# Kernel optimization log

Measured on AMD Instinct MI355X. Metric: run time of the kernel, lower is better.

The kernel has to match this reference:

```python
import jax, jax.numpy as jnp
import numpy as np

L = 4      # temporal transformer layers
H = 8      # heads
D = 512    # d_model (CLIP ViT-B/32 output dim)
FF = 2048  # feedforward dim
Q = 32     # query_pad_length
NEXP = 2   # visual expansion tokens
EPS = 1e-5


def _l2norm(x):
    n = jnp.linalg.norm(x, axis=-1, keepdims=True)
    return x / jnp.maximum(n, 1e-12)


def _layer_norm(x, w, b):
    m = jnp.mean(x, axis=-1, keepdims=True)
    v = jnp.mean(jnp.square(x - m), axis=-1, keepdims=True)
    return (x - m) / jnp.sqrt(v + EPS) * w + b


def _encoder_layer(x, Wqkv, bqkv, Wo, bo, g1, c1, W1, b1, W2, b2, g2, c2):
    # PyTorch TransformerEncoderLayer, batch_first, post-norm, ReLU, eval mode.
    B, S, _ = x.shape
    dh = D // H
    qkv = x @ Wqkv.T + bqkv                      # [B,S,3D]
    q, k, v = jnp.split(qkv, 3, axis=-1)
    q = q.reshape(B, S, H, dh).transpose(0, 2, 1, 3)
    k = k.reshape(B, S, H, dh).transpose(0, 2, 1, 3)
    v = v.reshape(B, S, H, dh).transpose(0, 2, 1, 3)
    scores = jnp.einsum('bhqd,bhkd->bhqk', q, k) / jnp.sqrt(jnp.float32(dh))
    attn = jax.nn.softmax(scores, axis=-1)
    o = jnp.einsum('bhqk,bhkd->bhqd', attn, v).transpose(0, 2, 1, 3).reshape(B, S, D)
    o = o @ Wo.T + bo
    x = _layer_norm(x + o, g1, c1)
    ff = jax.nn.relu(x @ W1.T + b1) @ W2.T + b2
    x = _layer_norm(x + ff, g2, c2)
    return x


def setup_inputs() -> dict:
    key = jax.random.key(0)
    ks = jax.random.split(key, 8)
    B, F = 256, 30
    s = 0.02
    return {
        'text_features': jax.random.normal(ks[0], (B, D), dtype=jnp.float32),
        'frame_features': jax.random.normal(ks[1], (B, F, D), dtype=jnp.float32),
        'expansion_tokens': jax.random.normal(ks[2], (1, NEXP, D), dtype=jnp.float32) * s,
        'W_qkv': jax.random.normal(ks[3], (L, 3 * D, D), dtype=jnp.float32) * s,
        'b_qkv': jnp.zeros((L, 3 * D), jnp.float32),
        'W_o': jax.random.normal(ks[4], (L, D, D), dtype=jnp.float32) * s,
        'b_o': jnp.zeros((L, D), jnp.float32),
        'ln1_w': jnp.ones((L, D), jnp.float32),
        'ln1_b': jnp.zeros((L, D), jnp.float32),
        'W1': jax.random.normal(ks[5], (L, FF, D), dtype=jnp.float32) * s,
        'b1': jnp.zeros((L, FF), jnp.float32),
        'W2': jax.random.normal(ks[6], (L, D, FF), dtype=jnp.float32) * s,
        'b2': jnp.zeros((L, D), jnp.float32),
        'ln2_w': jnp.ones((L, D), jnp.float32),
        'ln2_b': jnp.zeros((L, D), jnp.float32),
    }


def reference(text_features, frame_features, expansion_tokens, W_qkv, b_qkv,
              W_o, b_o, ln1_w, ln1_b, W1, b1, W2, b2, ln2_w, ln2_b):
    B, F = frame_features.shape[0], frame_features.shape[1]
    # encode_query: expand pooled text feature to Q identical tokens, l2-normalize
    q_feats = _l2norm(jnp.broadcast_to(text_features[:, None, :], (B, Q, D)))
    # temporal encoder on [frames; expansion tokens]
    x = jnp.concatenate(
        [frame_features, jnp.broadcast_to(expansion_tokens, (B, NEXP, D))], axis=1)
    for l in range(L):
        x = _encoder_layer(x, W_qkv[l], b_qkv[l], W_o[l], b_o[l],
                           ln1_w[l], ln1_b[l], W1[l], b1[l], W2[l], b2[l],
                           ln2_w[l], ln2_b[l])
    frame_n = _l2norm(frame_features)   # [B,F,D]
    video_n = _l2norm(x)                # [B,F+NEXP,D]
    # pairwise ColBERT MaxSim: similarities[i,j] = MMS(query_i, video_j)
    sim_f = jnp.einsum('bqd,cfd->bcqf', q_feats, frame_n).max(axis=-1).mean(axis=-1)
    sim_v = jnp.einsum('bqd,cvd->bcqv', q_feats, video_n).max(axis=-1).mean(axis=-1)
    return (sim_f + sim_v, sim_f, sim_v)
```

## Files before the change

kernel.cpp:

```cpp
#include <hip/hip_runtime.h>
#include <math.h>

#define DM 512
#define NTOK_V 62

typedef _Float16 h16;
typedef __attribute__((ext_vector_type(8))) _Float16 h16x8;
typedef __attribute__((ext_vector_type(4))) float f32x4;

__device__ __forceinline__ void ldsload16(const void* g, void* l) {
    __builtin_amdgcn_global_load_lds(
        (const __attribute__((address_space(1))) unsigned int*)g,
        (__attribute__((address_space(3))) unsigned int*)l, 16, 0, 0);
}

__device__ __forceinline__ void xcd_swz(int& bx, int& by) {
    const int gx = gridDim.x, gy = gridDim.y;
    const int lin = blockIdx.x + gx * blockIdx.y;
    const int cpx = (gx * gy) >> 3;
    const int wg = (lin & 7) * cpx + (lin >> 3);
    bx = wg % gx;
    by = wg / gx;
}

__global__ __launch_bounds__(256) void k_cvt(const float* __restrict__ in,
                                             h16* __restrict__ outp, int n8) {
    int i = blockIdx.x * 256 + threadIdx.x;
    if (i >= n8) return;
    float4 a = ((const float4*)in)[i * 2];
    float4 b = ((const float4*)in)[i * 2 + 1];
    h16x8 h;
    h[0] = (h16)a.x; h[1] = (h16)a.y; h[2] = (h16)a.z; h[3] = (h16)a.w;
    h[4] = (h16)b.x; h[5] = (h16)b.y; h[6] = (h16)b.z; h[7] = (h16)b.w;
    ((h16x8*)outp)[i] = h;
}

__global__ __launch_bounds__(256) void k_concat_h(const float* __restrict__ frames,
                                                  const float* __restrict__ expt,
                                                  h16* __restrict__ X) {
    int row = blockIdx.x;
    int b = row >> 5, s = row & 31;
    int t = threadIdx.x;
    const float* src = (s < 30) ? (frames + ((size_t)(b * 30 + s)) * DM)
                                : (expt + (size_t)(s - 30) * DM);
    X[(size_t)row * DM + t]       = (h16)src[t];
    X[(size_t)row * DM + t + 256] = (h16)src[t + 256];
}

template<int MODE>
__global__ __launch_bounds__(512, 2) void k_g8(
        const h16* __restrict__ A, int lda,
        const h16* __restrict__ B, int ldb,
        const float* __restrict__ bias,
        h16* __restrict__ C, int ldc,
        int M, int N, int Keff) {
    __shared__ char smem[131072];
    const int t = threadIdx.x;
    const int w = t >> 6, lane = t & 63;
    const int wr = w >> 2, wc = w & 3;
    const int kc = lane >> 4, rr = lane & 15;
    int bx, by;
    xcd_swz(bx, by);
    const size_t row0 = (size_t)by * 256;
    const size_t col0 = (size_t)bx * 256;

    const h16* gA = A + (row0 + (w << 4) + rr) * (size_t)lda + (kc << 3);
    const h16* gB = B + (col0 + (w << 4) + rr) * (size_t)ldb + (kc << 3);

    f32x4 acc[8][4];
#pragma unroll
    for (int m = 0; m < 8; ++m)
#pragma unroll
        for (int n = 0; n < 4; ++n) acc[m][n] = (f32x4){0.f, 0.f, 0.f, 0.f};

    const int nt = Keff >> 6;

#define SB0 __builtin_amdgcn_sched_barrier(0);
#define STG_A(bs, h, jt) { char* d_ = smem + (bs)*65536 + (h)*16384 + (w << 10) + (lane << 4); \
        const h16* s_ = gA + (size_t)((h)*128) * lda + (size_t)(jt)*64; \
        ldsload16(s_, d_); ldsload16(s_ + 32, d_ + 8192); }
#define STG_B(bs, h, jt) { char* d_ = smem + (bs)*65536 + 32768 + (h)*16384 + (w << 10) + (lane << 4); \
        const h16* s_ = gB + (size_t)((h)*128) * ldb + (size_t)(jt)*64; \
        ldsload16(s_, d_); ldsload16(s_ + 32, d_ + 8192); }
#define MFMA16(mp, AF) { \
        __builtin_amdgcn_s_setprio(1); \
        _Pragma("unroll") for (int i = 0; i < 2; ++i) \
        _Pragma("unroll") for (int n = 0; n < 4; ++n) \
        _Pragma("unroll") for (int kk = 0; kk < 2; ++kk) \
            acc[(mp)*2 + i][n] = __builtin_amdgcn_mfma_f32_16x16x32_f16(AF[i][kk], bf[n][kk], acc[(mp)*2 + i][n], 0, 0, 0); \
        __builtin_amdgcn_s_setprio(0); SB0 }

    STG_A(0, 0, 0) STG_A(0, 1, 0) STG_B(0, 0, 0) STG_B(0, 1, 0)

    int cur = 0;
    for (int j = 0; j < nt; ++j) {
        const int nxt = cur ^ 1;
        if (j + 1 < nt) {
            STG_A(nxt, 0, j + 1)
            asm volatile("s_waitcnt vmcnt(2)" ::: "memory");
        } else {
            asm volatile("s_waitcnt vmcnt(0)" ::: "memory");
        }
        SB0
        __builtin_amdgcn_s_barrier();
        SB0
        const char* Ab = smem + cur * 65536 + wr * 16384;
        const char* Bb = smem + cur * 65536 + 32768 + (wc >> 1) * 16384;
        h16x8 bf[4][2];
#pragma unroll
        for (int n = 0; n < 4; ++n)
#pragma unroll
            for (int kk = 0; kk < 2; ++kk)
                bf[n][kk] = *(const h16x8*)(Bb + kk * 8192 + (((wc & 1) << 2) + n) * 1024 + (lane << 4));
        h16x8 a0[2][2];
#pragma unroll
        for (int i = 0; i < 2; ++i)
#pragma unroll
            for (int kk = 0; kk < 2; ++kk)
                a0[i][kk] = *(const h16x8*)(Ab + kk * 8192 + (0 + i) * 1024 + (lane << 4));
        asm volatile("s_waitcnt lgkmcnt(0)" ::: "memory");
        SB0
        MFMA16(0, a0)
        h16x8 a1[2][2];
#pragma unroll
        for (int i = 0; i < 2; ++i)
#pragma unroll
            for (int kk = 0; kk < 2; ++kk)
                a1[i][kk] = *(const h16x8*)(Ab + kk * 8192 + (2 + i) * 1024 + (lane << 4));
        if (j + 1 < nt) STG_A(nxt, 1, j + 1)
        asm volatile("s_waitcnt lgkmcnt(0)" ::: "memory");
        SB0
        __builtin_amdgcn_s_barrier();
        SB0
        MFMA16(1, a1)
        h16x8 a2[2][2];
#pragma unroll
        for (int i = 0; i < 2; ++i)
#pragma unroll
            for (int kk = 0; kk < 2; ++kk)
                a2[i][kk] = *(const h16x8*)(Ab + kk * 8192 + (4 + i) * 1024 + (lane << 4));
        if (j + 1 < nt) STG_B(nxt, 0, j + 1)
        asm volatile("s_waitcnt lgkmcnt(0)" ::: "memory");
        SB0
        __builtin_amdgcn_s_barrier();
        SB0
        MFMA16(2, a2)
        h16x8 a3[2][2];
#pragma unroll
        for (int i = 0; i < 2; ++i)
#pragma unroll
            for (int kk = 0; kk < 2; ++kk)
                a3[i][kk] = *(const h16x8*)(Ab + kk * 8192 + (6 + i) * 1024 + (lane << 4));
        if (j + 1 < nt) STG_B(nxt, 1, j + 1)
        asm volatile("s_waitcnt lgkmcnt(0)" ::: "memory");
        SB0
        __builtin_amdgcn_s_barrier();
        SB0
        MFMA16(3, a3)
        cur = nxt;
    }
#undef MFMA16
#undef STG_A
#undef STG_B
#undef SB0

    float bv[4];
#pragma unroll
    for (int n = 0; n < 4; ++n)
        bv[n] = bias ? bias[col0 + (wc << 6) + n * 16 + rr] : 0.f;
#pragma unroll
    for (int m = 0; m < 8; ++m) {
        size_t rbase = row0 + (wr << 7) + m * 16 + (kc << 2);
#pragma unroll
        for (int jj = 0; jj < 4; ++jj) {
            h16* rowp = C + (rbase + jj) * (size_t)ldc + col0 + (wc << 6) + rr;
#pragma unroll
            for (int n = 0; n < 4; ++n) {
                float v = acc[m][n][jj] + bv[n];
                if (MODE == 1) v = fmaxf(v, 0.f);
                rowp[n * 16] = (h16)v;
            }
        }
    }
}

__global__ __launch_bounds__(512, 2) void k_g8n(
        const h16* __restrict__ A, int lda,
        const h16* __restrict__ B, int ldb,
        h16* __restrict__ C, int ldc,
        int M, int N, int Keff) {
    __shared__ char smem[98304];
    const int t = threadIdx.x;
    const int w = t >> 6, lane = t & 63;
    const int wr = w >> 1, wc = w & 1;
    const int kc = lane >> 4, rr = lane & 15;
    int bx, by;
    xcd_swz(bx, by);
    const size_t row0 = (size_t)by * 256;
    const size_t col0 = (size_t)bx * 128;
    const int z = blockIdx.z;

    const h16* gA = A + (size_t)z * Keff + (row0 + (w << 4) + rr) * (size_t)lda + (kc << 3);
    const h16* gB = B + (size_t)z * Keff + (col0 + (w << 4) + rr) * (size_t)ldb + (kc << 3);
    h16* Cz = C + (size_t)z * (size_t)M * N;

    f32x4 acc[4][4];
#pragma unroll
    for (int m = 0; m < 4; ++m)
#pragma unroll
        for (int n = 0; n < 4; ++n) acc[m][n] = (f32x4){0.f, 0.f, 0.f, 0.f};

    const int nt = Keff >> 6;

#define SB0 __builtin_amdgcn_sched_barrier(0);
#define STG_A(bs, h, jt) { char* d_ = smem + (bs)*49152 + (h)*16384 + (w << 10) + (lane << 4); \
        const h16* s_ = gA + (size_t)((h)*128) * lda + (size_t)(jt)*64; \
        ldsload16(s_, d_); ldsload16(s_ + 32, d_ + 8192); }
#define STG_B(bs, jt) { char* d_ = smem + (bs)*49152 + 32768 + (w << 10) + (lane << 4); \
        const h16* s_ = gB + (size_t)(jt)*64; \
        ldsload16(s_, d_); ldsload16(s_ + 32, d_ + 8192); }
#define MFMA8(mp, AF) { \
        __builtin_amdgcn_s_setprio(1); \
        _Pragma("unroll") for (int n = 0; n < 4; ++n) \
        _Pragma("unroll") for (int kk = 0; kk < 2; ++kk) \
            acc[mp][n] = __builtin_amdgcn_mfma_f32_16x16x32_f16(AF[kk], bf[n][kk], acc[mp][n], 0, 0, 0); \
        __builtin_amdgcn_s_setprio(0); SB0 }
#define LDA_FRAG(dst, mp) { int g_ = (wr << 2) + (mp); \
        const char* p_ = smem + cur * 49152 + ((g_ >> 3) << 14) + ((g_ & 7) << 10) + (lane << 4); \
        _Pragma("unroll") for (int kk = 0; kk < 2; ++kk) \
            dst[kk] = *(const h16x8*)(p_ + kk * 8192); }

    STG_A(0, 0, 0) STG_A(0, 1, 0) STG_B(0, 0)

    int cur = 0;
    for (int j = 0; j < nt; ++j) {
        const int nxt = cur ^ 1;
        if (j + 1 < nt) {
            STG_A(nxt, 0, j + 1)
            asm volatile("s_waitcnt vmcnt(2)" ::: "memory");
        } else {
            asm volatile("s_waitcnt vmcnt(0)" ::: "memory");
        }
        SB0
        __builtin_amdgcn_s_barrier();
        SB0
        const char* Bb = smem + cur * 49152 + 32768;
        h16x8 bf[4][2];
#pragma unroll
        for (int n = 0; n < 4; ++n)
#pragma unroll
            for (int kk = 0; kk < 2; ++kk)
                bf[n][kk] = *(const h16x8*)(Bb + kk * 8192 + (((wc << 2) + n) << 10) + (lane << 4));
        h16x8 a0[2];
        LDA_FRAG(a0, 0)
        asm volatile("s_waitcnt lgkmcnt(0)" ::: "memory");
        SB0
        MFMA8(0, a0)
        h16x8 a1[2];
        LDA_FRAG(a1, 1)
        if (j + 1 < nt) STG_A(nxt, 1, j + 1)
        asm volatile("s_waitcnt lgkmcnt(0)" ::: "memory");
        SB0
        __builtin_amdgcn_s_barrier();
        SB0
        MFMA8(1, a1)
        h16x8 a2[2];
        LDA_FRAG(a2, 2)
        if (j + 1 < nt) STG_B(nxt, j + 1)
        asm volatile("s_waitcnt lgkmcnt(0)" ::: "memory");
        SB0
        __builtin_amdgcn_s_barrier();
        SB0
        MFMA8(2, a2)
        h16x8 a3[2];
        LDA_FRAG(a3, 3)
        asm volatile("s_waitcnt lgkmcnt(0)" ::: "memory");
        SB0
        __builtin_amdgcn_s_barrier();
        SB0
        MFMA8(3, a3)
        cur = nxt;
    }
#undef LDA_FRAG
#undef MFMA8
#undef STG_A
#undef STG_B
#undef SB0

#pragma unroll
    for (int m = 0; m < 4; ++m) {
        size_t rbase = row0 + (wr << 6) + m * 16 + (kc << 2);
#pragma unroll
        for (int jj = 0; jj < 4; ++jj) {
            h16* rowp = Cz + (rbase + jj) * (size_t)ldc + col0 + (wc << 6) + rr;
#pragma unroll
            for (int n = 0; n < 4; ++n)
                rowp[n * 16] = (h16)acc[m][n][jj];
        }
    }
}

template<int MODE>
__global__ __launch_bounds__(512, 4) void k_hgemm(
        const h16* __restrict__ A, int lda,
        const h16* __restrict__ B, int ldb,
        const float* __restrict__ bias,
        h16* __restrict__ C, int ldc,
        int M, int N, int Keff) {
    __shared__ char smem[49152];
    const int t = threadIdx.x;
    const int w = t >> 6, lane = t & 63;
    const int wr = w >> 2, wc = w & 3;
    const int kc = lane >> 4, rr = lane & 15;
    int bx, by;
    xcd_swz(bx, by);
    const size_t row0 = (size_t)by * 128;
    const size_t col0 = (size_t)bx * 128;

    const h16* gA = A + (row0 + (w << 4) + rr) * (size_t)lda + (kc << 3);
    const h16* gB = B + (col0 + (w << 4) + rr) * (size_t)ldb + (kc << 3);

    f32x4 acc[4][2];
#pragma unroll
    for (int m = 0; m < 4; ++m)
#pragma unroll
        for (int n = 0; n < 2; ++n) acc[m][n] = (f32x4){0.f, 0.f, 0.f, 0.f};

    const int nt = Keff >> 5;

#define SB0 __builtin_amdgcn_sched_barrier(0);
#define STAGE(step, slot) { char* sA_ = smem + ((slot) << 14) + (w << 10); \
        ldsload16(gA + (size_t)(step) * 32, sA_); \
        ldsload16(gB + (size_t)(step) * 32, sA_ + 8192); }
#define KSTEP(WAITLIT, slotR, DOSTAGE, stepW, slotW) { \
        asm volatile("s_waitcnt vmcnt(" WAITLIT ")" ::: "memory"); \
        SB0 \
        __builtin_amdgcn_s_barrier(); \
        SB0 \
        const char* bA = smem + ((slotR) << 14); \
        const char* bB = bA + 8192; \
        h16x8 af[4], bf[2]; \
        _Pragma("unroll") for (int m = 0; m < 4; ++m) \
            af[m] = *(const h16x8*)(bA + ((wr << 2) + m) * 1024 + lane * 16); \
        _Pragma("unroll") for (int n = 0; n < 2; ++n) \
            bf[n] = *(const h16x8*)(bB + ((wc << 1) + n) * 1024 + lane * 16); \
        asm volatile("s_waitcnt lgkmcnt(0)" ::: "memory"); \
        SB0 \
        if (DOSTAGE) STAGE(stepW, slotW) \
        __builtin_amdgcn_s_setprio(1); \
        _Pragma("unroll") for (int m = 0; m < 4; ++m) \
        _Pragma("unroll") for (int n = 0; n < 2; ++n) \
            acc[m][n] = __builtin_amdgcn_mfma_f32_16x16x32_f16(af[m], bf[n], acc[m][n], 0, 0, 0); \
        __builtin_amdgcn_s_setprio(0); \
        SB0 }

    STAGE(0, 0) STAGE(1, 1)
    int slotR = 0, slotW = 2;
    int it = 0;
    for (; it < nt - 2; ++it) {
        KSTEP("2", slotR, 1, it + 2, slotW)
        slotR = (slotR == 2) ? 0 : slotR + 1;
        slotW = (slotW == 2) ? 0 : slotW + 1;
    }
    KSTEP("2", slotR, 0, 0, 0)
    slotR = (slotR == 2) ? 0 : slotR + 1;
    KSTEP("0", slotR, 0, 0, 0)
#undef KSTEP
#undef STAGE
#undef SB0

#pragma unroll
    for (int n = 0; n < 2; ++n) {
        size_t col = col0 + (wc << 5) + n * 16 + rr;
#pragma unroll
        for (int m = 0; m < 4; ++m) {
            size_t rbase = row0 + (wr << 6) + m * 16 + (kc << 2);
#pragma unroll
            for (int j = 0; j < 4; ++j)
                C[(rbase + j) * (size_t)ldc + col] = (h16)acc[m][n][j];
        }
    }
}

__global__ __launch_bounds__(512, 1) void k_fattn(
        const h16* __restrict__ QKV,
        const h16* __restrict__ Wo,
        const float* __restrict__ bo,
        h16* __restrict__ X,
        const float* __restrict__ lw,
        const float* __restrict__ lb) {
    __shared__ char smem[131072];
    const int t = threadIdx.x;
    const int w = t >> 6, lane = t & 63;
    const int rr = lane & 15, kc = lane >> 4;
    const size_t b = blockIdx.x;
    const size_t row0 = b * 32;
    const h16* qkv = QKV + row0 * 1536;

#define SB0 __builtin_amdgcn_sched_barrier(0);
#pragma unroll
    for (int mat = 0; mat < 3; ++mat)
#pragma unroll
        for (int g = 0; g < 2; ++g)
#pragma unroll
            for (int q = 0; q < 2; ++q) {
                const h16* src = qkv + (size_t)(g * 16 + rr) * 1536 + mat * 512 + w * 64 + q * 32 + kc * 8;
                ldsload16(src, smem + w * 12288 + mat * 4096 + (g * 2 + q) * 1024 + lane * 16);
            }
    asm volatile("s_waitcnt vmcnt(4)" ::: "memory");
    SB0

    const char* Qb = smem + w * 12288;
    const char* Kb = Qb + 4096;
    f32x4 s[2][2];
#pragma unroll
    for (int m = 0; m < 2; ++m)
#pragma unroll
        for (int n = 0; n < 2; ++n) s[m][n] = (f32x4){0.f, 0.f, 0.f, 0.f};
#pragma unroll
    for (int q = 0; q < 2; ++q) {
        h16x8 aq[2], bk[2];
#pragma unroll
        for (int m = 0; m < 2; ++m) aq[m] = *(const h16x8*)(Qb + (m * 2 + q) * 1024 + lane * 16);
#pragma unroll
        for (int n = 0; n < 2; ++n) bk[n] = *(const h16x8*)(Kb + (n * 2 + q) * 1024 + lane * 16);
#pragma unroll
        for (int m = 0; m < 2; ++m)
#pragma unroll
            for (int n = 0; n < 2; ++n)
                s[m][n] = __builtin_amdgcn_mfma_f32_16x16x32_f16(aq[m], bk[n], s[m][n], 0, 0, 0);
    }

    float p[2][2][4];
#pragma unroll
    for (int m = 0; m < 2; ++m)
#pragma unroll
        for (int j = 0; j < 4; ++j) {
            float a0 = s[m][0][j] * 0.125f, a1 = s[m][1][j] * 0.125f;
            float mx = fmaxf(a0, a1);
            mx = fmaxf(mx, __shfl_xor(mx, 1));
            mx = fmaxf(mx, __shfl_xor(mx, 2));
            mx = fmaxf(mx, __shfl_xor(mx, 4));
            mx = fmaxf(mx, __shfl_xor(mx, 8));
            float e0 = expf(a0 - mx), e1 = expf(a1 - mx);
            float sm = e0 + e1;
            sm += __shfl_xor(sm, 1);
            sm += __shfl_xor(sm, 2);
            sm += __shfl_xor(sm, 4);
            sm += __shfl_xor(sm, 8);
            float inv = 1.f / sm;
            p[m][0][j] = e0 * inv;
            p[m][1][j] = e1 * inv;
        }

    char* Pb = smem + 98304 + w * 2048;
#pragma unroll
    for (int m = 0; m < 2; ++m)
#pragma unroll
        for (int n = 0; n < 2; ++n)
#pragma unroll
            for (int j = 0; j < 4; ++j)
                *(h16*)(Pb + m * 1024 + (kc * 4 + j + ((n * 2 + (rr >> 3)) & 3) * 16) * 16 + (lane & 7) * 2) = (h16)p[m][n][j];
    asm volatile("s_waitcnt lgkmcnt(0)" ::: "memory");
    SB0
    h16x8 ap[2];
#pragma unroll
    for (int m = 0; m < 2; ++m) ap[m] = *(const h16x8*)(Pb + m * 1024 + lane * 16);

    asm volatile("s_waitcnt vmcnt(0)" ::: "memory");
    SB0

    const char* Vb = Qb + 8192;
    f32x4 o[2][4];
#pragma unroll
    for (int m = 0; m < 2; ++m)
#pragma unroll
        for (int n = 0; n < 4; ++n) o[m][n] = (f32x4){0.f, 0.f, 0.f, 0.f};
#pragma unroll
    for (int n = 0; n < 4; ++n) {
        h16x8 bv;
#pragma unroll
        for (int e = 0; e < 8; ++e)
            bv[e] = *(const h16*)(Vb + ((kc >> 1) * 2 + (n >> 1)) * 1024
                                  + ((kc & 1) * 8 + e) * 16
                                  + ((n * 2 + (rr >> 3)) & 3) * 256 + (lane & 7) * 2);
#pragma unroll
        for (int m = 0; m < 2; ++m)
            o[m][n] = __builtin_amdgcn_mfma_f32_16x16x32_f16(ap[m], bv, o[m][n], 0, 0, 0);
    }

#pragma unroll
    for (int m = 0; m < 2; ++m)
#pragma unroll
        for (int n = 0; n < 4; ++n)
#pragma unroll
            for (int j = 0; j < 4; ++j)
                *(h16*)(smem + 98304 + (m * 16 + w * 2 + (n >> 1)) * 1024
                        + (kc * 4 + j + ((n & 1) * 2 + (rr >> 3)) * 16) * 16 + (lane & 7) * 2) = (h16)o[m][n][j];
    asm volatile("s_waitcnt lgkmcnt(0)" ::: "memory");
    SB0
    __builtin_amdgcn_s_barrier();
    SB0

    f32x4 acc[2][4];
#pragma unroll
    for (int m = 0; m < 2; ++m)
#pragma unroll
        for (int n = 0; n < 4; ++n) acc[m][n] = (f32x4){0.f, 0.f, 0.f, 0.f};

#define STGB(js, sl) { _Pragma("unroll") for (int u = 0; u < 4; ++u) { \
        const h16* s_ = Wo + (size_t)((((u << 3) + w) << 4) + rr) * DM + (js) * 32 + (kc << 3); \
        ldsload16(s_, smem + (sl) * 32768 + (((u << 3) + w) << 10) + (lane << 4)); } }

    STGB(0, 0) STGB(1, 1)
    int slotR = 0, slotW = 2;
    for (int sx = 0; sx < 15; ++sx) {
        asm volatile("s_waitcnt vmcnt(4)" ::: "memory");
        SB0
        __builtin_amdgcn_s_barrier();
        SB0
        h16x8 af[2], bf[4];
#pragma unroll
        for (int m = 0; m < 2; ++m)
            af[m] = *(const h16x8*)(smem + 98304 + (m * 16 + sx) * 1024 + (lane << 4));
#pragma unroll
        for (int n = 0; n < 4; ++n)
            bf[n] = *(const h16x8*)(smem + slotR * 32768 + (((w << 2) + n) << 10) + (lane << 4));
        asm volatile("s_waitcnt lgkmcnt(0)" ::: "memory");
        SB0
        if (sx + 2 < 16) STGB(sx + 2, slotW)
        __builtin_amdgcn_s_setprio(1);
#pragma unroll
        for (int m = 0; m < 2; ++m)
#pragma unroll
            for (int n = 0; n < 4; ++n)
                acc[m][n] = __builtin_amdgcn_mfma_f32_16x16x32_f16(af[m], bf[n], acc[m][n], 0, 0, 0);
        __builtin_amdgcn_s_setprio(0);
        SB0
        slotR = (slotR == 2) ? 0 : slotR + 1;
        slotW = (slotW == 2) ? 0 : slotW + 1;
    }
    {
        asm volatile("s_waitcnt vmcnt(0)" ::: "memory");
        SB0
        __builtin_amdgcn_s_barrier();
        SB0
        h16x8 af[2], bf[4];
#pragma unroll
        for (int m = 0; m < 2; ++m)
            af[m] = *(const h16x8*)(smem + 98304 + (m * 16 + 15) * 1024 + (lane << 4));
#pragma unroll
        for (int n = 0; n < 4; ++n)
            bf[n] = *(const h16x8*)(smem + slotR * 32768 + (((w << 2) + n) << 10) + (lane << 4));
        asm volatile("s_waitcnt lgkmcnt(0)" ::: "memory");
        SB0
#pragma unroll
        for (int m = 0; m < 2; ++m)
#pragma unroll
            for (int n = 0; n < 4; ++n)
                acc[m][n] = __builtin_amdgcn_mfma_f32_16x16x32_f16(af[m], bf[n], acc[m][n], 0, 0, 0);
    }
#undef STGB
#undef SB0
    __syncthreads();

    float* outl = (float*)smem;
    float bvv[4];
#pragma unroll
    for (int n = 0; n < 4; ++n)
        bvv[n] = bo[(w << 6) + n * 16 + rr];
#pragma unroll
    for (int m = 0; m < 2; ++m)
#pragma unroll
        for (int n = 0; n < 4; ++n)
#pragma unroll
            for (int j = 0; j < 4; ++j) {
                int r = m * 16 + kc * 4 + j;
                int c = (w << 6) + n * 16 + rr;
                outl[r * 516 + c] = acc[m][n][j] + bvv[n];
            }
    __syncthreads();
    {
        const int r = t >> 4, l = t & 15;
        const size_t grow = (row0 + r) * (size_t)DM;
        float v[32];
        float sum = 0.f, sq = 0.f;
#pragma unroll
        for (int i = 0; i < 32; ++i) {
            int col = l + (i << 4);
            float vv = outl[r * 516 + col] + (float)X[grow + col];
            v[i] = vv;
            sum += vv;
            sq += vv * vv;
        }
#pragma unroll
        for (int o2 = 8; o2; o2 >>= 1) {
            sum += __shfl_xor(sum, o2);
            sq  += __shfl_xor(sq, o2);
        }
        float mean = sum * (1.f / 512.f);
        float var = sq * (1.f / 512.f) - mean * mean;
        float inv = 1.f / sqrtf(var + 1e-5f);
#pragma unroll
        for (int i = 0; i < 32; ++i) {
            int col = l + (i << 4);
            X[grow + col] = (h16)((v[i] - mean) * inv * lw[col] + lb[col]);
        }
    }
}

__global__ __launch_bounds__(256) void k_addln_red(h16* __restrict__ x,
                                                   const h16* __restrict__ p0,
                                                   const h16* __restrict__ p1,
                                                   const float* __restrict__ bias,
                                                   const float* __restrict__ w,
                                                   const float* __restrict__ b) {
    size_t row = blockIdx.x;
    int t = threadIdx.x;
    size_t o0 = row * DM + t, o1 = o0 + 256;
    float v0 = (float)x[o0] + (float)p0[o0] + (float)p1[o0] + bias[t];
    float v1 = (float)x[o1] + (float)p0[o1] + (float)p1[o1] + bias[t + 256];
    float s = v0 + v1;
#pragma unroll
    for (int o = 32; o; o >>= 1) s += __shfl_xor(s, o);
    __shared__ float ss[4], qs[4];
    if ((t & 63) == 0) ss[t >> 6] = s;
    __syncthreads();
    float mean = (ss[0] + ss[1] + ss[2] + ss[3]) * (1.f / 512.f);
    float d0 = v0 - mean, d1 = v1 - mean;
    float qv = d0 * d0 + d1 * d1;
#pragma unroll
    for (int o = 32; o; o >>= 1) qv += __shfl_xor(qv, o);
    if ((t & 63) == 0) qs[t >> 6] = qv;
    __syncthreads();
    float var = (qs[0] + qs[1] + qs[2] + qs[3]) * (1.f / 512.f);
    float inv = 1.f / sqrtf(var + 1e-5f);
    x[o0] = (h16)(d0 * inv * w[t] + b[t]);
    x[o1] = (h16)(d1 * inv * w[t + 256] + b[t + 256]);
}

__global__ __launch_bounds__(256) void k_l2rows_h(const float* __restrict__ in,
                                                  h16* __restrict__ outp) {
    size_t row = blockIdx.x;
    int t = threadIdx.x;
    float v0 = in[row * DM + t], v1 = in[row * DM + t + 256];
    float q = v0 * v0 + v1 * v1;
#pragma unroll
    for (int o = 32; o; o >>= 1) q += __shfl_xor(q, o);
    __shared__ float qs[4];
    if ((t & 63) == 0) qs[t >> 6] = q;
    __syncthreads();
    float n = sqrtf(qs[0] + qs[1] + qs[2] + qs[3]);
    float sc = 1.f / fmaxf(n, 1e-12f);
    outp[row * DM + t]       = (h16)(v0 * sc);
    outp[row * DM + t + 256] = (h16)(v1 * sc);
}

__global__ __launch_bounds__(256) void k_build_tok_h(const float* __restrict__ frames,
                                                     const h16* __restrict__ X,
                                                     h16* __restrict__ TOK) {
    int rid = blockIdx.x;
    int j = rid / NTOK_V, tt = rid % NTOK_V;
    int t = threadIdx.x;
    float v0, v1;
    if (tt < 30) {
        const float* src = frames + ((size_t)j * 30 + tt) * DM;
        v0 = src[t]; v1 = src[t + 256];
    } else {
        const h16* src = X + ((size_t)j * 32 + (tt - 30)) * DM;
        v0 = (float)src[t]; v1 = (float)src[t + 256];
    }
    float q = v0 * v0 + v1 * v1;
#pragma unroll
    for (int o = 32; o; o >>= 1) q += __shfl_xor(q, o);
    __shared__ float qs[4];
    if ((t & 63) == 0) qs[t >> 6] = q;
    __syncthreads();
    float n = sqrtf(qs[0] + qs[1] + qs[2] + qs[3]);
    float sc = 1.f / fmaxf(n, 1e-12f);
    TOK[(size_t)rid * DM + t]       = (h16)(v0 * sc);
    TOK[(size_t)rid * DM + t + 256] = (h16)(v1 * sc);
}

__global__ __launch_bounds__(256) void k_sim_h(const h16* __restrict__ dots,
                                               float* __restrict__ out) {
    int i = blockIdx.x;
    int j = threadIdx.x;
    const h16* p = dots + (size_t)i * 15872 + (size_t)j * NTOK_V;
    float mf = -1e30f, mv = -1e30f;
#pragma unroll
    for (int tt = 0; tt < 30; ++tt) mf = fmaxf(mf, (float)p[tt]);
#pragma unroll
    for (int tt = 30; tt < 62; ++tt) mv = fmaxf(mv, (float)p[tt]);
    int o = i * 256 + j;
    out[o]          = mf + mv;
    out[65536 + o]  = mf;
    out[131072 + o] = mv;
}

extern "C" void kernel_launch(void* const* d_in, const int* in_sizes, int n_in,
                              void* d_out, int out_size, void* d_ws, size_t ws_size,
                              hipStream_t stream) {
    const float* text   = (const float*)d_in[0];
    const float* frames = (const float*)d_in[1];
    const float* expt   = (const float*)d_in[2];
    const float* Wqkv   = (const float*)d_in[3];
    const float* bqkv   = (const float*)d_in[4];
    const float* Wo     = (const float*)d_in[5];
    const float* bo     = (const float*)d_in[6];
    const float* ln1w   = (const float*)d_in[7];
    const float* ln1b   = (const float*)d_in[8];
    const float* W1     = (const float*)d_in[9];
    const float* b1     = (const float*)d_in[10];
    const float* W2     = (const float*)d_in[11];
    const float* b2     = (const float*)d_in[12];
    const float* ln2w   = (const float*)d_in[13];
    const float* ln2b   = (const float*)d_in[14];
    float* out = (float*)d_out;

    char* wsb = (char*)d_ws;
    const size_t MB = 1024 * 1024;
    h16* Xh    = (h16*)(wsb);
    h16* P0    = (h16*)(wsb + 8 * MB);
    h16* P1    = (h16*)(wsb + 16 * MB);
    h16* FFh   = (h16*)(wsb + 32 * MB);
    h16* TOKh  = (h16*)(wsb + 32 * MB);
    h16* DOTSh = (h16*)(wsb + 48 * MB);
    h16* Wh    = (h16*)(wsb + 64 * MB);
    h16* QHATh = (h16*)(wsb + 90 * MB);

    h16* Whqkv = Wh;
    h16* Who   = Whqkv + 3145728;
    h16* Wh1   = Who + 1048576;
    h16* Wh2   = Wh1 + 4194304;

    k_cvt<<<1536, 256, 0, stream>>>(Wqkv, Whqkv, 393216);
    k_cvt<<<512,  256, 0, stream>>>(Wo,   Who,   131072);
    k_cvt<<<2048, 256, 0, stream>>>(W1,   Wh1,   524288);
    k_cvt<<<2048, 256, 0, stream>>>(W2,   Wh2,   524288);
    k_concat_h<<<8192, 256, 0, stream>>>(frames, expt, Xh);

    for (int l = 0; l < 4; ++l) {
        const h16* Wqkv_l = Whqkv + (size_t)l * 786432;
        const h16* Wo_l   = Who   + (size_t)l * 262144;
        const h16* W1_l   = Wh1   + (size_t)l * 1048576;
        const h16* W2_l   = Wh2   + (size_t)l * 1048576;

        k_g8<0><<<dim3(6, 32, 1), 512, 0, stream>>>(
            Xh, 512, Wqkv_l, 512, bqkv + (size_t)l * 1536, FFh, 1536, 8192, 1536, 512);
        k_fattn<<<256, 512, 0, stream>>>(FFh, Wo_l, bo + (size_t)l * 512, Xh,
                                         ln1w + (size_t)l * 512, ln1b + (size_t)l * 512);
        k_g8<1><<<dim3(8, 32, 1), 512, 0, stream>>>(
            Xh, 512, W1_l, 512, b1 + (size_t)l * 2048, FFh, 2048, 8192, 2048, 512);
        k_g8n<<<dim3(4, 32, 2), 512, 0, stream>>>(
            FFh, 2048, W2_l, 2048, P0, 512, 8192, 512, 1024);
        k_addln_red<<<8192, 256, 0, stream>>>(Xh, P0, P1, b2 + (size_t)l * 512,
                                              ln2w + (size_t)l * 512, ln2b + (size_t)l * 512);
    }

    k_l2rows_h<<<256, 256, 0, stream>>>(text, QHATh);
    k_build_tok_h<<<256 * NTOK_V, 256, 0, stream>>>(frames, Xh, TOKh);
    k_hgemm<2><<<dim3(124, 2, 1), 512, 0, stream>>>(
        QHATh, 512, TOKh, 512, nullptr, DOTSh, 15872, 256, 15872, 512);
    k_sim_h<<<256, 256, 0, stream>>>(DOTSh, out);
}
```

Before: 516.0 us.

## Split fused attention+Wo across head halves and move LayerNorm to reduction kernel

The fused attention kernel is split into two blocks per 32-row tile, each handling 4 heads and the matching half of the Wo K-dimension. Each half writes its fp16 partial output projection to a separate buffer, and the existing add+LayerNorm reduction kernel sums the two partials with bias and residual. The aim is twice as many blocks with lower LDS and thread counts (256 threads, two blocks per CU) so the 256-block launch fills the GPU better. The cost is an extra kernel launch, a round trip of partials through global memory, and fp16 rounding of the partial sums.

Result: slower. 546.8 us (+6.0%).

```diff
diff --git a/kernel.cpp b/kernel.cpp
--- a/kernel.cpp
+++ b/kernel.cpp
@@ -382,19 +382,17 @@
     }
 }
 
-__global__ __launch_bounds__(512, 1) void k_fattn(
+__global__ __launch_bounds__(256, 2) void k_fattn2(
         const h16* __restrict__ QKV,
         const h16* __restrict__ Wo,
-        const float* __restrict__ bo,
-        h16* __restrict__ X,
-        const float* __restrict__ lw,
-        const float* __restrict__ lb) {
-    __shared__ char smem[131072];
+        h16* __restrict__ Pp) {
+    __shared__ char smem[81920];
     const int t = threadIdx.x;
     const int w = t >> 6, lane = t & 63;
     const int rr = lane & 15, kc = lane >> 4;
-    const size_t b = blockIdx.x;
-    const size_t row0 = b * 32;
+    const int z = blockIdx.y;
+    const int hd = z * 4 + w;
+    const size_t row0 = (size_t)blockIdx.x * 32;
     const h16* qkv = QKV + row0 * 1536;
 
 #define SB0 __builtin_amdgcn_sched_barrier(0);
@@ -404,7 +402,7 @@
         for (int g = 0; g < 2; ++g)
 #pragma unroll
             for (int q = 0; q < 2; ++q) {
-                const h16* src = qkv + (size_t)(g * 16 + rr) * 1536 + mat * 512 + w * 64 + q * 32 + kc * 8;
+                const h16* src = qkv + (size_t)(g * 16 + rr) * 1536 + mat * 512 + hd * 64 + q * 32 + kc * 8;
                 ldsload16(src, smem + w * 12288 + mat * 4096 + (g * 2 + q) * 1024 + lane * 16);
             }
     asm volatile("s_waitcnt vmcnt(4)" ::: "memory");
@@ -453,14 +451,14 @@
             p[m][1][j] = e1 * inv;
         }
 
-    char* Pb = smem + 98304 + w * 2048;
+    char* Pb = smem + 65536 + w * 2048;
 #pragma unroll
     for (int m = 0; m < 2; ++m)
 #pragma unroll
         for (int n = 0; n < 2; ++n)
 #pragma unroll
             for (int j = 0; j < 4; ++j)
-                *(h16*)(Pb + m * 1024 + (kc * 4 + j + ((n * 2 + (rr >> 3)) & 3) * 16) * 16 + (lane & 7) * 2) = (h16)p[m][n][j];
+                *(h16*)(Pb + m * 1024 + (kc * 4 + j + (n * 2 + (rr >> 3)) * 16) * 16 + (lane & 7) * 2) = (h16)p[m][n][j];
     asm volatile("s_waitcnt lgkmcnt(0)" ::: "memory");
     SB0
     h16x8 ap[2];
@@ -495,118 +493,70 @@
         for (int n = 0; n < 4; ++n)
 #pragma unroll
             for (int j = 0; j < 4; ++j)
-                *(h16*)(smem + 98304 + (m * 16 + w * 2 + (n >> 1)) * 1024
+                *(h16*)(smem + 65536 + (m * 8 + w * 2 + (n >> 1)) * 1024
                         + (kc * 4 + j + ((n & 1) * 2 + (rr >> 3)) * 16) * 16 + (lane & 7) * 2) = (h16)o[m][n][j];
     asm volatile("s_waitcnt lgkmcnt(0)" ::: "memory");
     SB0
     __builtin_amdgcn_s_barrier();
     SB0
 
-    f32x4 acc[2][4];
+    f32x4 acc[2][8];
 #pragma unroll
     for (int m = 0; m < 2; ++m)
 #pragma unroll
-        for (int n = 0; n < 4; ++n) acc[m][n] = (f32x4){0.f, 0.f, 0.f, 0.f};
-
-#define STGB(js, sl) { _Pragma("unroll") for (int u = 0; u < 4; ++u) { \
-        const h16* s_ = Wo + (size_t)((((u << 3) + w) << 4) + rr) * DM + (js) * 32 + (kc << 3); \
-        ldsload16(s_, smem + (sl) * 32768 + (((u << 3) + w) << 10) + (lane << 4)); } }
+        for (int n = 0; n < 8; ++n) acc[m][n] = (f32x4){0.f, 0.f, 0.f, 0.f};
+
+#define STGB(js, sl) { _Pragma("unroll") for (int u = 0; u < 8; ++u) { \
+        const h16* s_ = Wo + (size_t)(u * 64 + (w << 4) + rr) * DM + z * 256 + (js) * 32 + (kc << 3); \
+        ldsload16(s_, smem + (sl) * 32768 + ((u * 4 + w) << 10) + (lane << 4)); } }
 
     STGB(0, 0) STGB(1, 1)
-    int slotR = 0, slotW = 2;
-    for (int sx = 0; sx < 15; ++sx) {
-        asm volatile("s_waitcnt vmcnt(4)" ::: "memory");
-        SB0
-        __builtin_amdgcn_s_barrier();
-        SB0
-        h16x8 af[2], bf[4];
+#pragma unroll
+    for (int sx = 0; sx < 8; ++sx) {
+        if (sx < 7) {
+            asm volatile("s_waitcnt vmcnt(8)" ::: "memory");
+        } else {
+            asm volatile("s_waitcnt vmcnt(0)" ::: "memory");
+        }
+        SB0
+        __builtin_amdgcn_s_barrier();
+        SB0
+        h16x8 af[2], bf[8];
 #pragma unroll
         for (int m = 0; m < 2; ++m)
-            af[m] = *(const h16x8*)(smem + 98304 + (m * 16 + sx) * 1024 + (lane << 4));
-#pragma unroll
-        for (int n = 0; n < 4; ++n)
-            bf[n] = *(const h16x8*)(smem + slotR * 32768 + (((w << 2) + n) << 10) + (lane << 4));
-        asm volatile("s_waitcnt lgkmcnt(0)" ::: "memory");
-        SB0
-        if (sx + 2 < 16) STGB(sx + 2, slotW)
+            af[m] = *(const h16x8*)(smem + 65536 + (m * 8 + sx) * 1024 + (lane << 4));
+#pragma unroll
+        for (int n = 0; n < 8; ++n)
+            bf[n] = *(const h16x8*)(smem + (sx & 1) * 32768 + ((w * 8 + n) << 10) + (lane << 4));
+        asm volatile("s_waitcnt lgkmcnt(0)" ::: "memory");
+        SB0
+        if (sx < 6) {
+            __builtin_amdgcn_s_barrier();
+            SB0
+            STGB(sx + 2, (sx & 1))
+        }
         __builtin_amdgcn_s_setprio(1);
 #pragma unroll
         for (int m = 0; m < 2; ++m)
 #pragma unroll
-            for (int n = 0; n < 4; ++n)
+            for (int n = 0; n < 8; ++n)
                 acc[m][n] = __builtin_amdgcn_mfma_f32_16x16x32_f16(af[m], bf[n], acc[m][n], 0, 0, 0);
         __builtin_amdgcn_s_setprio(0);
         SB0
-        slotR = (slotR == 2) ? 0 : slotR + 1;
-        slotW = (slotW == 2) ? 0 : slotW + 1;
-    }
-    {
-        asm volatile("s_waitcnt vmcnt(0)" ::: "memory");
-        SB0
-        __builtin_amdgcn_s_barrier();
-        SB0
-        h16x8 af[2], bf[4];
-#pragma unroll
-        for (int m = 0; m < 2; ++m)
-            af[m] = *(const h16x8*)(smem + 98304 + (m * 16 + 15) * 1024 + (lane << 4));
-#pragma unroll
-        for (int n = 0; n < 4; ++n)
-            bf[n] = *(const h16x8*)(smem + slotR * 32768 + (((w << 2) + n) << 10) + (lane << 4));
-        asm volatile("s_waitcnt lgkmcnt(0)" ::: "memory");
-        SB0
-#pragma unroll
-        for (int m = 0; m < 2; ++m)
-#pragma unroll
-            for (int n = 0; n < 4; ++n)
-                acc[m][n] = __builtin_amdgcn_mfma_f32_16x16x32_f16(af[m], bf[n], acc[m][n], 0, 0, 0);
     }
 #undef STGB
 #undef SB0
-    __syncthreads();
-
-    float* outl = (float*)smem;
-    float bvv[4];
-#pragma unroll
-    for (int n = 0; n < 4; ++n)
-        bvv[n] = bo[(w << 6) + n * 16 + rr];
+
+    h16* Pz = Pp + (size_t)z * 4194304;
 #pragma unroll
     for (int m = 0; m < 2; ++m)
 #pragma unroll
-        for (int n = 0; n < 4; ++n)
-#pragma unroll
-            for (int j = 0; j < 4; ++j) {
-                int r = m * 16 + kc * 4 + j;
-                int c = (w << 6) + n * 16 + rr;
-                outl[r * 516 + c] = acc[m][n][j] + bvv[n];
-            }
-    __syncthreads();
-    {
-        const int r = t >> 4, l = t & 15;
-        const size_t grow = (row0 + r) * (size_t)DM;
-        float v[32];
-        float sum = 0.f, sq = 0.f;
-#pragma unroll
-        for (int i = 0; i < 32; ++i) {
-            int col = l + (i << 4);
-            float vv = outl[r * 516 + col] + (float)X[grow + col];
-            v[i] = vv;
-            sum += vv;
-            sq += vv * vv;
-        }
-#pragma unroll
-        for (int o2 = 8; o2; o2 >>= 1) {
-            sum += __shfl_xor(sum, o2);
-            sq  += __shfl_xor(sq, o2);
-        }
-        float mean = sum * (1.f / 512.f);
-        float var = sq * (1.f / 512.f) - mean * mean;
-        float inv = 1.f / sqrtf(var + 1e-5f);
-#pragma unroll
-        for (int i = 0; i < 32; ++i) {
-            int col = l + (i << 4);
-            X[grow + col] = (h16)((v[i] - mean) * inv * lw[col] + lb[col]);
-        }
-    }
+        for (int jj = 0; jj < 4; ++jj) {
+            h16* rowp = Pz + (row0 + m * 16 + kc * 4 + jj) * (size_t)DM + (w << 7) + rr;
+#pragma unroll
+            for (int n = 0; n < 8; ++n)
+                rowp[n * 16] = (h16)acc[m][n][jj];
+        }
 }
 
 __global__ __launch_bounds__(256) void k_addln_red(h16* __restrict__ x,
@@ -748,8 +698,9 @@
 
         k_g8<0><<<dim3(6, 32, 1), 512, 0, stream>>>(
             Xh, 512, Wqkv_l, 512, bqkv + (size_t)l * 1536, FFh, 1536, 8192, 1536, 512);
-        k_fattn<<<256, 512, 0, stream>>>(FFh, Wo_l, bo + (size_t)l * 512, Xh,
-                                         ln1w + (size_t)l * 512, ln1b + (size_t)l * 512);
+        k_fattn2<<<dim3(256, 2), 256, 0, stream>>>(FFh, Wo_l, P0);
+        k_addln_red<<<8192, 256, 0, stream>>>(Xh, P0, P1, bo + (size_t)l * 512,
+                                              ln1w + (size_t)l * 512, ln1b + (size_t)l * 512);
         k_g8<1><<<dim3(8, 32, 1), 512, 0, stream>>>(
             Xh, 512, W1_l, 512, b1 + (size_t)l * 2048, FFh, 2048, 8192, 2048, 512);
         k_g8n<<<dim3(4, 32, 2), 512, 0, stream>>>(
```
